# Kernel tuning notes

Measured on AMD Instinct MI355X. Metric: run time of the kernel, lower is better.

Reference implementation:

```python
import jax, jax.numpy as jnp
import numpy as np

HEADS = 8
DIM_HEAD = 64
GROUPS = 32
GN_EPS = 1e-5


def setup_inputs() -> dict:
    key = jax.random.key(0)
    ks = jax.random.split(key, 6)
    B, D, CD, T = 8, 256, 256, 8192
    H = HEADS * DIM_HEAD  # 512
    return {
        "x": jax.random.normal(ks[0], (B, D, T), jnp.float32),
        "cs": jax.random.normal(ks[1], (B, CD, T), jnp.float32),
        "Wq": jax.random.normal(ks[2], (H, D), jnp.float32) * (1.0 / np.sqrt(D)),
        "Wkv": jax.random.normal(ks[3], (2 * H, CD), jnp.float32) * (1.0 / np.sqrt(CD)),
        "Wout": jax.random.normal(ks[4], (D, H), jnp.float32) * (1.0 / np.sqrt(H)),
        "bout": jax.random.normal(ks[5], (D,), jnp.float32) * 0.01,
        "gn_gamma": jnp.ones((D,), jnp.float32),
        "gn_beta": jnp.zeros((D,), jnp.float32),
    }


def reference(x, cs, Wq, Wkv, Wout, bout, gn_gamma, gn_beta):
    B, D, T = x.shape
    scale = DIM_HEAD ** -0.5

    # 1x1 conv projections == channel matmuls
    q = jnp.einsum('od,bdt->bot', Wq, x)            # [B, H*C, T]
    kv = jnp.einsum('od,bdt->bot', Wkv, cs)         # [B, 2*H*C, T]
    k, v = jnp.split(kv, 2, axis=1)

    # b (h c) t -> b h c t
    q = q.reshape(B, HEADS, DIM_HEAD, T)
    k = k.reshape(B, HEADS, DIM_HEAD, T)
    v = v.reshape(B, HEADS, DIM_HEAD, T)

    q = jax.nn.softmax(q, axis=-2) * scale          # softmax over head-dim
    k = jax.nn.softmax(k, axis=-1)                  # softmax over time

    # context: [B, H, d, e] (tiny d_head x d_head)
    context = jnp.einsum('bhdn,bhen->bhde', k, v)
    out = jnp.einsum('bhde,bhdn->bhen', context, q)  # [B, H, d_head, T]
    out = out.reshape(B, HEADS * DIM_HEAD, T)

    # output 1x1 conv (with bias) + GroupNorm(32, D)
    y = jnp.einsum('od,bdt->bot', Wout, out) + bout[None, :, None]
    g = y.reshape(B, GROUPS, D // GROUPS, T)
    mean = g.mean(axis=(2, 3), keepdims=True)
    var = g.var(axis=(2, 3), keepdims=True)
    g = (g - mean) * jax.lax.rsqrt(var + GN_EPS)
    y = g.reshape(B, D, T) * gn_gamma[None, :, None] + gn_beta[None, :, None]
    return y
```

## Files before the change

### kernel.cpp

```cpp
#include <hip/hip_runtime.h>
#include <math.h>

#define T_DIM 8192
#define B_DIM 8
#define D_DIM 256
#define CD_DIM 256
#define HC 512
#define NHEAD 8
#define CHEAD 64
#define NGROUP 32
#define GN_EPS 1e-5f
#define QSCALE 0.125f

#define CHUNK_OFF   0ull
#define KST_OFF     2097152ull
#define CTX_OFF     2129920ull
#define GNS_OFF     3178496ull
#define GNQ_OFF     3179520ull
#define GNM_OFF     3180544ull
#define GNR_OFF     3181568ull
#define MM_OFF      3182592ull
#define ZERO_FLOATS 262656

__global__ __launch_bounds__(256) void k_zero(float* __restrict__ p, int n) {
  int i = blockIdx.x * 256 + threadIdx.x;
  if (i < n) p[i] = 0.f;
}

__global__ __launch_bounds__(256) void k_kchunk(const float* __restrict__ Wkv,
                                                const float* __restrict__ cs,
                                                float* __restrict__ chunkstats) {
  __shared__ float As[32][132];
  __shared__ float Bs[32][132];
  __shared__ float Rm[128][17];
  __shared__ float Rs[128][17];
  __shared__ float Ms[128];

  const int tid = threadIdx.x;
  const int tx = tid & 15, ty = tid >> 4;
  const int chunk = blockIdx.x;
  const int t0 = chunk * 128;
  const int rb = blockIdx.y * 128;
  const int b = blockIdx.z;

  float acc[8][8];
#pragma unroll
  for (int i = 0; i < 8; ++i)
#pragma unroll
    for (int j = 0; j < 8; ++j) acc[i][j] = 0.f;

  for (int k0 = 0; k0 < CD_DIM; k0 += 32) {
    for (int idx = tid; idx < 128 * 32; idx += 256) {
      int r = idx >> 5, kk = idx & 31;
      As[kk][r] = Wkv[(rb + r) * CD_DIM + k0 + kk];
    }
    for (int idx = tid; idx < 32 * 128; idx += 256) {
      int kk = idx >> 7, c = idx & 127;
      Bs[kk][c] = cs[(b * CD_DIM + k0 + kk) * T_DIM + t0 + c];
    }
    __syncthreads();
#pragma unroll
    for (int kk = 0; kk < 32; ++kk) {
      const float4 a0 = *reinterpret_cast<const float4*>(&As[kk][ty * 8]);
      const float4 a1 = *reinterpret_cast<const float4*>(&As[kk][ty * 8 + 4]);
      const float4 b0 = *reinterpret_cast<const float4*>(&Bs[kk][tx * 8]);
      const float4 b1 = *reinterpret_cast<const float4*>(&Bs[kk][tx * 8 + 4]);
      const float av[8] = {a0.x, a0.y, a0.z, a0.w, a1.x, a1.y, a1.z, a1.w};
      const float bv[8] = {b0.x, b0.y, b0.z, b0.w, b1.x, b1.y, b1.z, b1.w};
#pragma unroll
      for (int i = 0; i < 8; ++i)
#pragma unroll
        for (int j = 0; j < 8; ++j) acc[i][j] = fmaf(av[i], bv[j], acc[i][j]);
    }
    __syncthreads();
  }

#pragma unroll
  for (int i = 0; i < 8; ++i) {
    float pm = acc[i][0];
#pragma unroll
    for (int j = 1; j < 8; ++j) pm = fmaxf(pm, acc[i][j]);
    Rm[ty * 8 + i][tx] = pm;
  }
  __syncthreads();
  if (tid < 128) {
    float m = Rm[tid][0];
#pragma unroll
    for (int jj = 1; jj < 16; ++jj) m = fmaxf(m, Rm[tid][jj]);
    Ms[tid] = m;
  }
  __syncthreads();
#pragma unroll
  for (int i = 0; i < 8; ++i) {
    const float m = Ms[ty * 8 + i];
    float ps = 0.f;
#pragma unroll
    for (int j = 0; j < 8; ++j) ps += __expf(acc[i][j] - m);
    Rs[ty * 8 + i][tx] = ps;
  }
  __syncthreads();
  if (tid < 128) {
    float s = 0.f;
#pragma unroll
    for (int jj = 0; jj < 16; ++jj) s += Rs[tid][jj];
    const size_t o = ((size_t)(b * HC + rb + tid) * 64 + chunk) * 2;
    chunkstats[o] = Ms[tid];
    chunkstats[o + 1] = s;
  }
}

__global__ __launch_bounds__(64) void k_kcomb(const float* __restrict__ chunkstats,
                                              float* __restrict__ kstats) {
  const int r = blockIdx.x;
  const int b = blockIdx.y;
  const int lane = threadIdx.x;
  const size_t o = ((size_t)(b * HC + r) * 64 + lane) * 2;
  float m = chunkstats[o];
  float s = chunkstats[o + 1];
#pragma unroll
  for (int off = 32; off > 0; off >>= 1) {
    float m2 = __shfl_xor(m, off);
    float s2 = __shfl_xor(s, off);
    float mn = fmaxf(m, m2);
    s = s * __expf(m - mn) + s2 * __expf(m2 - mn);
    m = mn;
  }
  if (lane == 0) {
    kstats[(b * HC + r) * 2] = m;
    kstats[(b * HC + r) * 2 + 1] = 1.f / s;
  }
}

__global__ __launch_bounds__(256) void k_ctx2(const float* __restrict__ Wkv,
                                              const float* __restrict__ cs,
                                              const float* __restrict__ kstats,
                                              float* __restrict__ ctx) {
  __shared__ float Wk[32][68];
  __shared__ float Wv[32][68];
  __shared__ float Cs[32][68];
  __shared__ float Ks[64][68];
  __shared__ float Vs[64][68];

  const int tid = threadIdx.x;
  const int tx = tid & 15, ty = tid >> 4;
  const int tc0 = blockIdx.x * 1024;
  const int h = blockIdx.y;
  const int b = blockIdx.z;

  float msr[4], zsr[4];
#pragma unroll
  for (int i = 0; i < 4; ++i) {
    msr[i] = kstats[(b * HC + h * CHEAD + ty * 4 + i) * 2];
    zsr[i] = kstats[(b * HC + h * CHEAD + ty * 4 + i) * 2 + 1];
  }

  float cacc[4][4];
#pragma unroll
  for (int i = 0; i < 4; ++i)
#pragma unroll
    for (int j = 0; j < 4; ++j) cacc[i][j] = 0.f;

  for (int sc = 0; sc < 16; ++sc) {
    const int t0 = tc0 + sc * 64;
    float ka[4][4], va[4][4];
#pragma unroll
    for (int i = 0; i < 4; ++i)
#pragma unroll
      for (int j = 0; j < 4; ++j) { ka[i][j] = 0.f; va[i][j] = 0.f; }

    for (int k0 = 0; k0 < CD_DIM; k0 += 32) {
      __syncthreads();
      for (int idx = tid; idx < 32 * 64; idx += 256) {
        int kk = idx & 31, r = idx >> 5;
        Wk[kk][r] = Wkv[(h * CHEAD + r) * CD_DIM + k0 + kk];
        Wv[kk][r] = Wkv[(HC + h * CHEAD + r) * CD_DIM + k0 + kk];
        int kk2 = idx >> 6, r2 = idx & 63;
        Cs[kk2][r2] = cs[(b * CD_DIM + k0 + kk2) * T_DIM + t0 + r2];
      }
      __syncthreads();
#pragma unroll
      for (int kk = 0; kk < 32; ++kk) {
        const float4 a4 = *reinterpret_cast<const float4*>(&Wk[kk][ty * 4]);
        const float4 w4 = *reinterpret_cast<const float4*>(&Wv[kk][ty * 4]);
        const float4 c4 = *reinterpret_cast<const float4*>(&Cs[kk][tx * 4]);
        const float av[4] = {a4.x, a4.y, a4.z, a4.w};
        const float wv[4] = {w4.x, w4.y, w4.z, w4.w};
        const float cv[4] = {c4.x, c4.y, c4.z, c4.w};
#pragma unroll
        for (int i = 0; i < 4; ++i)
#pragma unroll
          for (int j = 0; j < 4; ++j) {
            ka[i][j] = fmaf(av[i], cv[j], ka[i][j]);
            va[i][j] = fmaf(wv[i], cv[j], va[i][j]);
          }
      }
    }
    __syncthreads();
#pragma unroll
    for (int i = 0; i < 4; ++i)
#pragma unroll
      for (int j = 0; j < 4; ++j) {
        Ks[tx * 4 + j][ty * 4 + i] = __expf(ka[i][j] - msr[i]) * zsr[i];
        Vs[tx * 4 + j][ty * 4 + i] = va[i][j];
      }
    __syncthreads();
#pragma unroll 8
    for (int tt = 0; tt < 64; ++tt) {
      const float4 kd = *reinterpret_cast<const float4*>(&Ks[tt][ty * 4]);
      const float4 ve = *reinterpret_cast<const float4*>(&Vs[tt][tx * 4]);
      const float kv_[4] = {kd.x, kd.y, kd.z, kd.w};
      const float vv[4] = {ve.x, ve.y, ve.z, ve.w};
#pragma unroll
      for (int i = 0; i < 4; ++i)
#pragma unroll
        for (int j = 0; j < 4; ++j) cacc[i][j] = fmaf(kv_[i], vv[j], cacc[i][j]);
    }
  }
#pragma unroll
  for (int i = 0; i < 4; ++i)
#pragma unroll
    for (int j = 0; j < 4; ++j)
      atomicAdd(&ctx[((size_t)(b * NHEAD + h) * CHEAD + ty * 4 + i) * CHEAD + tx * 4 + j],
                cacc[i][j]);
}

__global__ __launch_bounds__(256) void k_mmat(const float* __restrict__ Wout,
                                              const float* __restrict__ ctx,
                                              float* __restrict__ Mm) {
  __shared__ float Ws[64][65];
  __shared__ float Csh[64][65];
  const int tid = threadIdx.x;
  const int o0 = blockIdx.x * 64;
  const int h = blockIdx.y;
  const int b = blockIdx.z;

  for (int idx = tid; idx < 4096; idx += 256) {
    int r = idx >> 6, e = idx & 63;
    Ws[e][r] = Wout[(o0 + r) * HC + h * CHEAD + e];
    Csh[e][r] = ctx[((size_t)(b * NHEAD + h) * CHEAD + r) * CHEAD + e];
  }
  __syncthreads();
  const int tx = tid & 15, ty = tid >> 4;
  float acc[4][4];
#pragma unroll
  for (int i = 0; i < 4; ++i)
#pragma unroll
    for (int j = 0; j < 4; ++j) acc[i][j] = 0.f;
#pragma unroll 16
  for (int e = 0; e < 64; ++e) {
    float av[4], bv[4];
#pragma unroll
    for (int i = 0; i < 4; ++i) av[i] = Ws[e][ty * 4 + i];
#pragma unroll
    for (int j = 0; j < 4; ++j) bv[j] = Csh[e][tx * 4 + j];
#pragma unroll
    for (int i = 0; i < 4; ++i)
#pragma unroll
      for (int j = 0; j < 4; ++j) acc[i][j] = fmaf(av[i], bv[j], acc[i][j]);
  }
#pragma unroll
  for (int i = 0; i < 4; ++i)
#pragma unroll
    for (int j = 0; j < 4; ++j)
      Mm[(size_t)(b * D_DIM + o0 + ty * 4 + i) * HC + h * CHEAD + tx * 4 + j] = acc[i][j];
}

__global__ __launch_bounds__(256, 3) void k_fused_y(const float* __restrict__ Wq,
                                                    const float* __restrict__ x,
                                                    const float* __restrict__ Mm,
                                                    const float* __restrict__ bout,
                                                    float* __restrict__ out,
                                                    float* __restrict__ gnsum,
                                                    float* __restrict__ gnsumsq) {
  __shared__ float Wx[64][68];
  __shared__ float Xs[64][68];
  __shared__ float Qs[64][68];

  const int tid = threadIdx.x;
  const int tx = tid & 15, ty = tid >> 4;
  const int t0 = blockIdx.x * 64;
  const int b = blockIdx.y;

  const int wkk = tid & 63;
  const int wr0 = tid >> 6;
  const int xcq = tid & 15;
  const int xk0 = tid >> 4;

  float yacc[16][4];
#pragma unroll
  for (int i = 0; i < 16; ++i)
#pragma unroll
    for (int j = 0; j < 4; ++j) yacc[i][j] = 0.f;

  float wq[16];
  float4 xv[4];

  for (int h = 0; h < NHEAD; ++h) {
    float qa[4][4];
#pragma unroll
    for (int i = 0; i < 4; ++i)
#pragma unroll
      for (int j = 0; j < 4; ++j) qa[i][j] = 0.f;

    {
      const float* wp = Wq + (size_t)(h * CHEAD + wr0) * D_DIM + wkk;
#pragma unroll
      for (int t = 0; t < 16; ++t) wq[t] = wp[(size_t)t * 4 * D_DIM];
      const float* xp = x + ((size_t)b * D_DIM + xk0) * T_DIM + t0 + xcq * 4;
#pragma unroll
      for (int t = 0; t < 4; ++t)
        xv[t] = *reinterpret_cast<const float4*>(xp + (size_t)t * 16 * T_DIM);
    }

    for (int kc = 0; kc < 4; ++kc) {
#pragma unroll
      for (int t = 0; t < 16; ++t) Wx[wkk][wr0 + 4 * t] = wq[t];
#pragma unroll
      for (int t = 0; t < 4; ++t)
        *reinterpret_cast<float4*>(&Xs[xk0 + 16 * t][xcq * 4]) = xv[t];
      __syncthreads();

      if (kc < 3) {
        const int k0 = (kc + 1) * 64;
        const float* wp = Wq + (size_t)(h * CHEAD + wr0) * D_DIM + k0 + wkk;
#pragma unroll
        for (int t = 0; t < 16; ++t) wq[t] = wp[(size_t)t * 4 * D_DIM];
        const float* xp = x + ((size_t)b * D_DIM + k0 + xk0) * T_DIM + t0 + xcq * 4;
#pragma unroll
        for (int t = 0; t < 4; ++t)
          xv[t] = *reinterpret_cast<const float4*>(xp + (size_t)t * 16 * T_DIM);
      }

#pragma unroll 16
      for (int kk = 0; kk < 64; ++kk) {
        const float4 a4 = *reinterpret_cast<const float4*>(&Wx[kk][ty * 4]);
        const float4 c4 = *reinterpret_cast<const float4*>(&Xs[kk][tx * 4]);
        const float av[4] = {a4.x, a4.y, a4.z, a4.w};
        const float cv[4] = {c4.x, c4.y, c4.z, c4.w};
#pragma unroll
        for (int i = 0; i < 4; ++i)
#pragma unroll
          for (int j = 0; j < 4; ++j) qa[i][j] = fmaf(av[i], cv[j], qa[i][j]);
      }
      __syncthreads();
    }

#pragma unroll
    for (int i = 0; i < 4; ++i)
      *reinterpret_cast<float4*>(&Qs[ty * 4 + i][tx * 4]) =
          make_float4(qa[i][0], qa[i][1], qa[i][2], qa[i][3]);
    __syncthreads();

    {
      const int c = tid & 63;
      const int qt = tid >> 6;
      float pm = -1e30f;
#pragma unroll
      for (int r = 0; r < 16; ++r) pm = fmaxf(pm, Qs[qt * 16 + r][c]);
      Xs[qt][c] = pm;
      __syncthreads();
      const float m = fmaxf(fmaxf(Xs[0][c], Xs[1][c]), fmaxf(Xs[2][c], Xs[3][c]));
      float ps = 0.f;
#pragma unroll
      for (int r = 0; r < 16; ++r) {
        const float e = __expf(Qs[qt * 16 + r][c] - m);
        Qs[qt * 16 + r][c] = e;
        ps += e;
      }
      Xs[8 + qt][c] = ps;
      __syncthreads();
      const float s4 = Xs[8][c] + Xs[9][c] + Xs[10][c] + Xs[11][c];
      const float inv = QSCALE / s4;
#pragma unroll
      for (int r = 0; r < 16; ++r) Qs[qt * 16 + r][c] *= inv;
      __syncthreads();
    }

    {
      const float* Mb = Mm + (size_t)b * D_DIM * HC + h * CHEAD;
#pragma unroll 4
      for (int d0 = 0; d0 < 64; d0 += 4) {
        const float4 q0 = *reinterpret_cast<const float4*>(&Qs[d0 + 0][tx * 4]);
        const float4 q1 = *reinterpret_cast<const float4*>(&Qs[d0 + 1][tx * 4]);
        const float4 q2 = *reinterpret_cast<const float4*>(&Qs[d0 + 2][tx * 4]);
        const float4 q3 = *reinterpret_cast<const float4*>(&Qs[d0 + 3][tx * 4]);
#pragma unroll
        for (int i = 0; i < 16; ++i) {
          const float4 m4 =
              *reinterpret_cast<const float4*>(Mb + (size_t)(ty + 16 * i) * HC + d0);
          yacc[i][0] = fmaf(m4.x, q0.x, fmaf(m4.y, q1.x, fmaf(m4.z, q2.x, fmaf(m4.w, q3.x, yacc[i][0]))));
          yacc[i][1] = fmaf(m4.x, q0.y, fmaf(m4.y, q1.y, fmaf(m4.z, q2.y, fmaf(m4.w, q3.y, yacc[i][1]))));
          yacc[i][2] = fmaf(m4.x, q0.z, fmaf(m4.y, q1.z, fmaf(m4.z, q2.z, fmaf(m4.w, q3.z, yacc[i][2]))));
          yacc[i][3] = fmaf(m4.x, q0.w, fmaf(m4.y, q1.w, fmaf(m4.z, q2.w, fmaf(m4.w, q3.w, yacc[i][3]))));
        }
      }
    }
  }

#pragma unroll
  for (int i = 0; i < 16; ++i) {
    const int row = ty + 16 * i;
    const float bias = bout[row];
    float s = 0.f, qq = 0.f;
#pragma unroll
    for (int j = 0; j < 4; ++j) {
      yacc[i][j] += bias;
      s += yacc[i][j];
      qq += yacc[i][j] * yacc[i][j];
    }
    *reinterpret_cast<float4*>(&out[(size_t)(b * D_DIM + row) * T_DIM + t0 + tx * 4]) =
        make_float4(yacc[i][0], yacc[i][1], yacc[i][2], yacc[i][3]);
#pragma unroll
    for (int off = 1; off <= 8; off <<= 1) {
      s += __shfl_xor(s, off);
      qq += __shfl_xor(qq, off);
    }
    s += __shfl_xor(s, 16); qq += __shfl_xor(qq, 16);
    s += __shfl_xor(s, 32); qq += __shfl_xor(qq, 32);
    if ((tid & 63) == 0) {
      const int g = 2 * i + (tid >> 7);
      atomicAdd(&gnsum[b * NGROUP + g], s);
      atomicAdd(&gnsumsq[b * NGROUP + g], qq);
    }
  }
}

__global__ void k_gnfin(const float* __restrict__ gnsum, const float* __restrict__ gnsumsq,
                        float* __restrict__ gnmean, float* __restrict__ gnrs) {
  const int tid = threadIdx.x;
  const float cnt = (float)((D_DIM / NGROUP) * T_DIM);
  float mean = gnsum[tid] / cnt;
  float var = gnsumsq[tid] / cnt - mean * mean;
  gnmean[tid] = mean;
  gnrs[tid] = rsqrtf(var + GN_EPS);
}

__global__ __launch_bounds__(256) void k_apply(float* __restrict__ out,
                                               const float* __restrict__ gnmean,
                                               const float* __restrict__ gnrs,
                                               const float* __restrict__ gamma,
                                               const float* __restrict__ beta) {
  const int n4 = (B_DIM * D_DIM * T_DIM) / 4;
  for (int i = blockIdx.x * 256 + threadIdx.x; i < n4; i += gridDim.x * 256) {
    float4 v = reinterpret_cast<const float4*>(out)[i];
    const int row = i >> 11;
    const int c = row & (D_DIM - 1);
    const int b = row >> 8;
    const int gi = b * NGROUP + (c >> 3);
    const float a = gnrs[gi] * gamma[c];
    const float bb = beta[c] - gnmean[gi] * a;
    v.x = v.x * a + bb; v.y = v.y * a + bb; v.z = v.z * a + bb; v.w = v.w * a + bb;
    reinterpret_cast<float4*>(out)[i] = v;
  }
}

extern "C" void kernel_launch(void* const* d_in, const int* in_sizes, int n_in,
                              void* d_out, int out_size, void* d_ws, size_t ws_size,
                              hipStream_t stream) {
  const float* x     = (const float*)d_in[0];
  const float* cs    = (const float*)d_in[1];
  const float* Wq    = (const float*)d_in[2];
  const float* Wkv   = (const float*)d_in[3];
  const float* Wout  = (const float*)d_in[4];
  const float* bout  = (const float*)d_in[5];
  const float* gamma = (const float*)d_in[6];
  const float* beta  = (const float*)d_in[7];
  float* out = (float*)d_out;
  char* ws = (char*)d_ws;

  float* chunkstats = (float*)(ws + CHUNK_OFF);
  float* kstats     = (float*)(ws + KST_OFF);
  float* ctx        = (float*)(ws + CTX_OFF);
  float* gnsum      = (float*)(ws + GNS_OFF);
  float* gnsumsq    = (float*)(ws + GNQ_OFF);
  float* gnmean     = (float*)(ws + GNM_OFF);
  float* gnrs       = (float*)(ws + GNR_OFF);
  float* Mm         = (float*)(ws + MM_OFF);

  k_zero   <<<(ZERO_FLOATS + 255) / 256, 256, 0, stream>>>(ctx, ZERO_FLOATS);
  k_kchunk <<<dim3(64, 4, 8), 256, 0, stream>>>(Wkv, cs, chunkstats);
  k_kcomb  <<<dim3(512, 8),   64,  0, stream>>>(chunkstats, kstats);
  k_ctx2   <<<dim3(8, 8, 8),  256, 0, stream>>>(Wkv, cs, kstats, ctx);
  k_mmat   <<<dim3(4, 8, 8),  256, 0, stream>>>(Wout, ctx, Mm);
  k_fused_y<<<dim3(128, 8),   256, 0, stream>>>(Wq, x, Mm, bout, out, gnsum, gnsumsq);
  k_gnfin  <<<1, 256, 0, stream>>>(gnsum, gnsumsq, gnmean, gnrs);
  k_apply  <<<4096, 256, 0, stream>>>(out, gnmean, gnrs, gamma, beta);
}
```

Before: 2.026 ms.

## Halve fused_y time tile, keep x in LDS, read Wq from global directly

The fused Q-projection/output kernel now handles 32 time columns per block instead of 64, which doubles the grid to 2048 blocks and raises the occupancy hint to 4. The whole 256x32 x tile is loaded into shared memory once and reused across all 8 heads. Wq rows are read straight from global/cache as float4 instead of being staged through shared memory. The head-dim softmax reduction now uses wave shuffles instead of shared-memory round trips and extra barriers. In exchange, each thread does half the work per output, Mm and Wq reads are repeated across twice as many blocks, and the Wq global reads are uncoalesced broadcasts.

```diff
diff --git a/kernel.cpp b/kernel.cpp
--- a/kernel.cpp
+++ b/kernel.cpp
@@ -265,133 +265,114 @@
       Mm[(size_t)(b * D_DIM + o0 + ty * 4 + i) * HC + h * CHEAD + tx * 4 + j] = acc[i][j];
 }
 
-__global__ __launch_bounds__(256, 3) void k_fused_y(const float* __restrict__ Wq,
+__global__ __launch_bounds__(256, 4) void k_fused_y(const float* __restrict__ Wq,
                                                     const float* __restrict__ x,
                                                     const float* __restrict__ Mm,
                                                     const float* __restrict__ bout,
                                                     float* __restrict__ out,
                                                     float* __restrict__ gnsum,
                                                     float* __restrict__ gnsumsq) {
-  __shared__ float Wx[64][68];
-  __shared__ float Xs[64][68];
-  __shared__ float Qs[64][68];
+  __shared__ float Xs[256][32];
+  __shared__ float Qs[64][32];
 
   const int tid = threadIdx.x;
   const int tx = tid & 15, ty = tid >> 4;
-  const int t0 = blockIdx.x * 64;
+  const int t0 = blockIdx.x * 32;
   const int b = blockIdx.y;
 
-  const int wkk = tid & 63;
-  const int wr0 = tid >> 6;
-  const int xcq = tid & 15;
-  const int xk0 = tid >> 4;
-
-  float yacc[16][4];
-#pragma unroll
-  for (int i = 0; i < 16; ++i)
-#pragma unroll
-    for (int j = 0; j < 4; ++j) yacc[i][j] = 0.f;
-
-  float wq[16];
-  float4 xv[4];
+  {
+    const int cq = tid & 7, r0 = tid >> 3;
+    const float* xp = x + ((size_t)b * D_DIM + r0) * T_DIM + t0 + cq * 4;
+#pragma unroll
+    for (int r = 0; r < 8; ++r)
+      *reinterpret_cast<float4*>(&Xs[r0 + 32 * r][cq * 4]) =
+          *reinterpret_cast<const float4*>(xp + (size_t)r * 32 * T_DIM);
+  }
+  __syncthreads();
+
+  float yacc[16][2];
+#pragma unroll
+  for (int i = 0; i < 16; ++i) { yacc[i][0] = 0.f; yacc[i][1] = 0.f; }
 
   for (int h = 0; h < NHEAD; ++h) {
-    float qa[4][4];
+    float qa[4][2];
+#pragma unroll
+    for (int i = 0; i < 4; ++i) { qa[i][0] = 0.f; qa[i][1] = 0.f; }
+    const float* Wh = Wq + (size_t)h * CHEAD * D_DIM;
+#pragma unroll 4
+    for (int k0 = 0; k0 < D_DIM; k0 += 4) {
+      float4 w[4];
+#pragma unroll
+      for (int i = 0; i < 4; ++i)
+        w[i] = *reinterpret_cast<const float4*>(Wh + (size_t)(ty * 4 + i) * D_DIM + k0);
+      float2 xr[4];
+#pragma unroll
+      for (int kk = 0; kk < 4; ++kk)
+        xr[kk] = *reinterpret_cast<const float2*>(&Xs[k0 + kk][tx * 2]);
+#pragma unroll
+      for (int i = 0; i < 4; ++i) {
+        qa[i][0] = fmaf(w[i].x, xr[0].x, qa[i][0]);
+        qa[i][0] = fmaf(w[i].y, xr[1].x, qa[i][0]);
+        qa[i][0] = fmaf(w[i].z, xr[2].x, qa[i][0]);
+        qa[i][0] = fmaf(w[i].w, xr[3].x, qa[i][0]);
+        qa[i][1] = fmaf(w[i].x, xr[0].y, qa[i][1]);
+        qa[i][1] = fmaf(w[i].y, xr[1].y, qa[i][1]);
+        qa[i][1] = fmaf(w[i].z, xr[2].y, qa[i][1]);
+        qa[i][1] = fmaf(w[i].w, xr[3].y, qa[i][1]);
+      }
+    }
+
+    __syncthreads();
 #pragma unroll
     for (int i = 0; i < 4; ++i)
-#pragma unroll
-      for (int j = 0; j < 4; ++j) qa[i][j] = 0.f;
+      *reinterpret_cast<float2*>(&Qs[ty * 4 + i][tx * 2]) = make_float2(qa[i][0], qa[i][1]);
+    __syncthreads();
 
     {
-      const float* wp = Wq + (size_t)(h * CHEAD + wr0) * D_DIM + wkk;
-#pragma unroll
-      for (int t = 0; t < 16; ++t) wq[t] = wp[(size_t)t * 4 * D_DIM];
-      const float* xp = x + ((size_t)b * D_DIM + xk0) * T_DIM + t0 + xcq * 4;
-#pragma unroll
-      for (int t = 0; t < 4; ++t)
-        xv[t] = *reinterpret_cast<const float4*>(xp + (size_t)t * 16 * T_DIM);
-    }
-
-    for (int kc = 0; kc < 4; ++kc) {
-#pragma unroll
-      for (int t = 0; t < 16; ++t) Wx[wkk][wr0 + 4 * t] = wq[t];
-#pragma unroll
-      for (int t = 0; t < 4; ++t)
-        *reinterpret_cast<float4*>(&Xs[xk0 + 16 * t][xcq * 4]) = xv[t];
-      __syncthreads();
-
-      if (kc < 3) {
-        const int k0 = (kc + 1) * 64;
-        const float* wp = Wq + (size_t)(h * CHEAD + wr0) * D_DIM + k0 + wkk;
-#pragma unroll
-        for (int t = 0; t < 16; ++t) wq[t] = wp[(size_t)t * 4 * D_DIM];
-        const float* xp = x + ((size_t)b * D_DIM + k0 + xk0) * T_DIM + t0 + xcq * 4;
-#pragma unroll
-        for (int t = 0; t < 4; ++t)
-          xv[t] = *reinterpret_cast<const float4*>(xp + (size_t)t * 16 * T_DIM);
-      }
-
-#pragma unroll 16
-      for (int kk = 0; kk < 64; ++kk) {
-        const float4 a4 = *reinterpret_cast<const float4*>(&Wx[kk][ty * 4]);
-        const float4 c4 = *reinterpret_cast<const float4*>(&Xs[kk][tx * 4]);
-        const float av[4] = {a4.x, a4.y, a4.z, a4.w};
-        const float cv[4] = {c4.x, c4.y, c4.z, c4.w};
-#pragma unroll
-        for (int i = 0; i < 4; ++i)
-#pragma unroll
-          for (int j = 0; j < 4; ++j) qa[i][j] = fmaf(av[i], cv[j], qa[i][j]);
-      }
-      __syncthreads();
-    }
-
-#pragma unroll
-    for (int i = 0; i < 4; ++i)
-      *reinterpret_cast<float4*>(&Qs[ty * 4 + i][tx * 4]) =
-          make_float4(qa[i][0], qa[i][1], qa[i][2], qa[i][3]);
-    __syncthreads();
-
-    {
-      const int c = tid & 63;
-      const int qt = tid >> 6;
+      const int c = tid >> 3;
+      const int qt = tid & 7;
       float pm = -1e30f;
 #pragma unroll
-      for (int r = 0; r < 16; ++r) pm = fmaxf(pm, Qs[qt * 16 + r][c]);
-      Xs[qt][c] = pm;
-      __syncthreads();
-      const float m = fmaxf(fmaxf(Xs[0][c], Xs[1][c]), fmaxf(Xs[2][c], Xs[3][c]));
+      for (int r = 0; r < 8; ++r) pm = fmaxf(pm, Qs[qt * 8 + r][c]);
+      pm = fmaxf(pm, __shfl_xor(pm, 1));
+      pm = fmaxf(pm, __shfl_xor(pm, 2));
+      pm = fmaxf(pm, __shfl_xor(pm, 4));
       float ps = 0.f;
 #pragma unroll
-      for (int r = 0; r < 16; ++r) {
-        const float e = __expf(Qs[qt * 16 + r][c] - m);
-        Qs[qt * 16 + r][c] = e;
+      for (int r = 0; r < 8; ++r) {
+        const float e = __expf(Qs[qt * 8 + r][c] - pm);
+        Qs[qt * 8 + r][c] = e;
         ps += e;
       }
-      Xs[8 + qt][c] = ps;
-      __syncthreads();
-      const float s4 = Xs[8][c] + Xs[9][c] + Xs[10][c] + Xs[11][c];
-      const float inv = QSCALE / s4;
-#pragma unroll
-      for (int r = 0; r < 16; ++r) Qs[qt * 16 + r][c] *= inv;
-      __syncthreads();
-    }
+      ps += __shfl_xor(ps, 1);
+      ps += __shfl_xor(ps, 2);
+      ps += __shfl_xor(ps, 4);
+      const float inv = QSCALE / ps;
+#pragma unroll
+      for (int r = 0; r < 8; ++r) Qs[qt * 8 + r][c] *= inv;
+    }
+    __syncthreads();
 
     {
       const float* Mb = Mm + (size_t)b * D_DIM * HC + h * CHEAD;
 #pragma unroll 4
       for (int d0 = 0; d0 < 64; d0 += 4) {
-        const float4 q0 = *reinterpret_cast<const float4*>(&Qs[d0 + 0][tx * 4]);
-        const float4 q1 = *reinterpret_cast<const float4*>(&Qs[d0 + 1][tx * 4]);
-        const float4 q2 = *reinterpret_cast<const float4*>(&Qs[d0 + 2][tx * 4]);
-        const float4 q3 = *reinterpret_cast<const float4*>(&Qs[d0 + 3][tx * 4]);
+        const float2 q0 = *reinterpret_cast<const float2*>(&Qs[d0 + 0][tx * 2]);
+        const float2 q1 = *reinterpret_cast<const float2*>(&Qs[d0 + 1][tx * 2]);
+        const float2 q2 = *reinterpret_cast<const float2*>(&Qs[d0 + 2][tx * 2]);
+        const float2 q3 = *reinterpret_cast<const float2*>(&Qs[d0 + 3][tx * 2]);
 #pragma unroll
         for (int i = 0; i < 16; ++i) {
           const float4 m4 =
               *reinterpret_cast<const float4*>(Mb + (size_t)(ty + 16 * i) * HC + d0);
-          yacc[i][0] = fmaf(m4.x, q0.x, fmaf(m4.y, q1.x, fmaf(m4.z, q2.x, fmaf(m4.w, q3.x, yacc[i][0]))));
-          yacc[i][1] = fmaf(m4.x, q0.y, fmaf(m4.y, q1.y, fmaf(m4.z, q2.y, fmaf(m4.w, q3.y, yacc[i][1]))));
-          yacc[i][2] = fmaf(m4.x, q0.z, fmaf(m4.y, q1.z, fmaf(m4.z, q2.z, fmaf(m4.w, q3.z, yacc[i][2]))));
-          yacc[i][3] = fmaf(m4.x, q0.w, fmaf(m4.y, q1.w, fmaf(m4.z, q2.w, fmaf(m4.w, q3.w, yacc[i][3]))));
+          yacc[i][0] = fmaf(m4.x, q0.x, yacc[i][0]);
+          yacc[i][0] = fmaf(m4.y, q1.x, yacc[i][0]);
+          yacc[i][0] = fmaf(m4.z, q2.x, yacc[i][0]);
+          yacc[i][0] = fmaf(m4.w, q3.x, yacc[i][0]);
+          yacc[i][1] = fmaf(m4.x, q0.y, yacc[i][1]);
+          yacc[i][1] = fmaf(m4.y, q1.y, yacc[i][1]);
+          yacc[i][1] = fmaf(m4.z, q2.y, yacc[i][1]);
+          yacc[i][1] = fmaf(m4.w, q3.y, yacc[i][1]);
         }
       }
     }
@@ -401,15 +382,12 @@
   for (int i = 0; i < 16; ++i) {
     const int row = ty + 16 * i;
     const float bias = bout[row];
-    float s = 0.f, qq = 0.f;
-#pragma unroll
-    for (int j = 0; j < 4; ++j) {
-      yacc[i][j] += bias;
-      s += yacc[i][j];
-      qq += yacc[i][j] * yacc[i][j];
-    }
-    *reinterpret_cast<float4*>(&out[(size_t)(b * D_DIM + row) * T_DIM + t0 + tx * 4]) =
-        make_float4(yacc[i][0], yacc[i][1], yacc[i][2], yacc[i][3]);
+    yacc[i][0] += bias;
+    yacc[i][1] += bias;
+    float s = yacc[i][0] + yacc[i][1];
+    float qq = yacc[i][0] * yacc[i][0] + yacc[i][1] * yacc[i][1];
+    *reinterpret_cast<float2*>(&out[(size_t)(b * D_DIM + row) * T_DIM + t0 + tx * 2]) =
+        make_float2(yacc[i][0], yacc[i][1]);
 #pragma unroll
     for (int off = 1; off <= 8; off <<= 1) {
       s += __shfl_xor(s, off);
@@ -482,7 +460,7 @@
   k_kcomb  <<<dim3(512, 8),   64,  0, stream>>>(chunkstats, kstats);
   k_ctx2   <<<dim3(8, 8, 8),  256, 0, stream>>>(Wkv, cs, kstats, ctx);
   k_mmat   <<<dim3(4, 8, 8),  256, 0, stream>>>(Wout, ctx, Mm);
-  k_fused_y<<<dim3(128, 8),   256, 0, stream>>>(Wq, x, Mm, bout, out, gnsum, gnsumsq);
+  k_fused_y<<<dim3(256, 8),   256, 0, stream>>>(Wq, x, Mm, bout, out, gnsum, gnsumsq);
   k_gnfin  <<<1, 256, 0, stream>>>(gnsum, gnsumsq, gnmean, gnrs);
   k_apply  <<<4096, 256, 0, stream>>>(out, gnmean, gnrs, gamma, beta);
 }
```

New measurement: 2.526 ms. +24.7%, slower.
